# Kernel tuning notes

Hardware: AMD Instinct MI355X
Metric: run time of the kernel (lower is better)

## Reference

```python
import jax, jax.numpy as jnp
import numpy as np

N = 50000
E = 800000
H, C = 8, 16          # heads, per-head channels (H*C = 128)
G = 64                # number of graphs
EPS = 1e-5


def setup_inputs() -> dict:
    key = jax.random.key(0)
    ks = jax.random.split(key, 8)
    x = jax.random.normal(ks[0], (N, 128), dtype=jnp.float32)
    edge_index = jax.random.randint(ks[1], (2, E), 0, N, dtype=jnp.int64)
    batch = jnp.sort(jax.random.randint(ks[2], (N,), 0, G, dtype=jnp.int64))
    W = jax.random.normal(ks[3], (3, 128, 128), dtype=jnp.float32) * 0.08
    att_src = jax.random.normal(ks[4], (3, H, C), dtype=jnp.float32) * 0.1
    att_dst = jax.random.normal(ks[5], (3, H, C), dtype=jnp.float32) * 0.1
    bias = jnp.zeros((3, 128), dtype=jnp.float32)
    gamma = jnp.ones((3, 128), dtype=jnp.float32)
    beta = jnp.zeros((3, 128), dtype=jnp.float32)
    ro_w = jax.random.normal(ks[6], (128, 2), dtype=jnp.float32) * 0.08
    ro_b = jnp.zeros((2,), dtype=jnp.float32)
    return {"x": x, "edge_index": edge_index, "batch": batch, "W": W,
            "att_src": att_src, "att_dst": att_dst, "bias": bias,
            "gamma": gamma, "beta": beta, "ro_w": ro_w, "ro_b": ro_b}


def _gat_block(prev, h, src, dst, W, a_s, a_d, b, g, be):
    # GATConv (concat=True, add_self_loops already applied to src/dst)
    xp = (h @ W).reshape(N, H, C)                       # [N,H,C]
    al_s = jnp.sum(xp * a_s, axis=-1)                   # [N,H]
    al_d = jnp.sum(xp * a_d, axis=-1)                   # [N,H]
    logits = jax.nn.leaky_relu(al_s[src] + al_d[dst], negative_slope=0.2)  # [Et,H]
    m = jax.ops.segment_max(logits, dst, num_segments=N)        # softmax over dst groups
    ex = jnp.exp(logits - m[dst])
    denom = jax.ops.segment_sum(ex, dst, num_segments=N)
    alpha = ex / denom[dst]                              # [Et,H]
    msg = xp[src] * alpha[:, :, None]                    # [Et,H,C]
    agg = jax.ops.segment_sum(msg, dst, num_segments=N).reshape(N, H * C) + b
    y = prev + agg
    # BatchNorm1d (training mode: batch stats, biased variance)
    mu = y.mean(axis=0)
    var = y.var(axis=0)
    yn = (y - mu) / jnp.sqrt(var + EPS) * g + be
    return jax.nn.elu(yn)


def reference(x, edge_index, batch, W, att_src, att_dst, bias, gamma, beta, ro_w, ro_b):
    loops = jnp.arange(N, dtype=edge_index.dtype)
    src = jnp.concatenate([edge_index[0], loops])        # PyG add_self_loops=True
    dst = jnp.concatenate([edge_index[1], loops])
    h = x
    prev = jnp.zeros((N, 128), dtype=x.dtype)
    for i in range(3):
        out = _gat_block(prev, h, src, dst, W[i], att_src[i], att_dst[i],
                         bias[i], gamma[i], beta[i])
        prev = h[:, :128]
        h = out
    # global mean pool over graphs
    sums = jax.ops.segment_sum(h, batch, num_segments=G)
    cnt = jax.ops.segment_sum(jnp.ones((N,), dtype=h.dtype), batch, num_segments=G)
    pooled = sums / jnp.maximum(cnt, 1.0)[:, None]
    return pooled @ ro_w + ro_b
```

## Files before the change

### kernel.cpp

```cpp
#include <hip/hip_runtime.h>
#include <hip/hip_bf16.h>
#include <math.h>

#define NN 50000
#define EE 800000
#define MM (EE + NN)
#define GG 64
#define SWG 512
#define NSB ((NN + 255) / 256)
#define PSP 16

__device__ __forceinline__ int geti(const void* p, long idx, int is64) {
    return is64 ? (int)((const long long*)p)[idx] : ((const int*)p)[idx];
}

__device__ __forceinline__ float bf2f(unsigned short u) {
    return __uint_as_float(((unsigned)u) << 16);
}

__device__ __forceinline__ float eluf(float z) {
    return z > 0.f ? z : expm1f(z);
}

__global__ void k_detect(const int* __restrict__ ei, int* __restrict__ flag) {
    if (blockIdx.x == 0 && threadIdx.x == 0) {
        int ok = 1;
        for (int k = 0; k < 128; ++k) {
            int lo = ei[2 * k], hi = ei[2 * k + 1];
            if (hi != 0 || (unsigned)lo >= (unsigned)NN) { ok = 0; break; }
        }
        flag[0] = ok;
    }
}


__global__ void k_zero(int* p, int n) {
    int i = blockIdx.x * blockDim.x + threadIdx.x;
    if (i < n) p[i] = 0;
}

__global__ void k_count(const void* __restrict__ ei, const int* __restrict__ flag,
                        int* __restrict__ counts) {
    int e = blockIdx.x * blockDim.x + threadIdx.x;
    if (e >= MM) return;
    int is64 = flag[0];
    int d = (e < EE) ? geti(ei, (long)EE + e, is64) : (e - EE);
    if ((unsigned)d < (unsigned)NN) atomicAdd(&counts[d], 1);
}

__global__ __launch_bounds__(256) void k_scan1(const int* __restrict__ counts,
                                               int* __restrict__ rowptr,
                                               int* __restrict__ bsum) {
    __shared__ int buf[256];
    int b = blockIdx.x, tid = threadIdx.x;
    int i = b * 256 + tid;
    int v = (i < NN) ? counts[i] : 0;
    buf[tid] = v;
    __syncthreads();
    for (int off = 1; off < 256; off <<= 1) {
        int t = (tid >= off) ? buf[tid - off] : 0;
        __syncthreads();
        buf[tid] += t;
        __syncthreads();
    }
    if (i < NN) rowptr[i + 1] = buf[tid];
    if (tid == 255) bsum[b] = buf[255];
}

__global__ __launch_bounds__(256) void k_scan2(int* __restrict__ bsum) {
    __shared__ int buf[256];
    int tid = threadIdx.x;
    int v = (tid < NSB) ? bsum[tid] : 0;
    buf[tid] = v;
    __syncthreads();
    for (int off = 1; off < 256; off <<= 1) {
        int t = (tid >= off) ? buf[tid - off] : 0;
        __syncthreads();
        buf[tid] += t;
        __syncthreads();
    }
    if (tid < NSB) bsum[tid] = (tid == 0) ? 0 : buf[tid - 1];
}

__global__ __launch_bounds__(256) void k_scan3(int* __restrict__ rowptr,
                                               const int* __restrict__ bsum) {
    int b = blockIdx.x, tid = threadIdx.x;
    int i = b * 256 + tid;
    if (i < NN) rowptr[i + 1] += bsum[b];
    if (b == 0 && tid == 0) rowptr[0] = 0;
}

__global__ void k_fill(const void* __restrict__ ei, const int* __restrict__ flag,
                       const int* __restrict__ rowptr,
                       int* __restrict__ fill, int* __restrict__ colv) {
    int e = blockIdx.x * blockDim.x + threadIdx.x;
    if (e >= MM) return;
    int is64 = flag[0];
    int s, d;
    if (e < EE) { s = geti(ei, e, is64); d = geti(ei, (long)EE + e, is64); }
    else { s = d = e - EE; }
    if ((unsigned)d >= (unsigned)NN || (unsigned)s >= (unsigned)NN) return;
    int pos = rowptr[d] + atomicAdd(&fill[d], 1);
    if ((unsigned)pos < (unsigned)MM) colv[pos] = s;
}


__global__ __launch_bounds__(256) void k_gemm_att(
    const float* __restrict__ hsrc, const float* __restrict__ Ysrc,
    const float* __restrict__ st, const float* __restrict__ W,
    const float* __restrict__ attS, const float* __restrict__ attD,
    unsigned short* __restrict__ xpb, float* __restrict__ als,
    float* __restrict__ ald, int n)
{
    __shared__ float Wt[32][8][12];
    __shared__ float Ht[128][33];
    int tid = threadIdx.x;
    int hh = tid & 7;
    int r0 = tid >> 3;
    int rbase = (blockIdx.x >> 1) * 128;
    int cbase = (blockIdx.x & 1) * 64;
    bool useY = (Ysrc != nullptr);

    float acc[4][8];
#pragma unroll
    for (int a = 0; a < 4; ++a)
#pragma unroll
        for (int b = 0; b < 8; ++b) acc[a][b] = 0.f;

    for (int k0 = 0; k0 < 128; k0 += 32) {
#pragma unroll
        for (int jj = 0; jj < 2; ++jj) {
            int idx = tid * 2 + jj;
            int kk = idx >> 4;
            int cpos = (idx & 15) * 4;
            int h2 = cpos >> 3, t = cpos & 7;
            *(float4*)&Wt[kk][h2][t] =
                *(const float4*)&W[(k0 + kk) * 128 + cbase + h2 * 8 + t];
        }
#pragma unroll
        for (int j = 0; j < 4; ++j) {
            int f = tid * 16 + j * 4;
            int r = f >> 5, kk = f & 31;
            int gr = rbase + r;
            float4 v = make_float4(0.f, 0.f, 0.f, 0.f);
            if (gr < n) {
                if (useY) {
                    float4 yv = *(const float4*)&Ysrc[gr * 128 + k0 + kk];
                    float4 scv = *(const float4*)&st[k0 + kk];
                    float4 shv = *(const float4*)&st[128 + k0 + kk];
                    v.x = eluf(fmaf(yv.x, scv.x, shv.x));
                    v.y = eluf(fmaf(yv.y, scv.y, shv.y));
                    v.z = eluf(fmaf(yv.z, scv.z, shv.z));
                    v.w = eluf(fmaf(yv.w, scv.w, shv.w));
                } else {
                    v = *(const float4*)&hsrc[gr * 128 + k0 + kk];
                }
            }
            Ht[r][kk] = v.x; Ht[r][kk + 1] = v.y; Ht[r][kk + 2] = v.z; Ht[r][kk + 3] = v.w;
        }
        __syncthreads();
#pragma unroll 4
        for (int kk = 0; kk < 32; ++kk) {
            float wv[8];
            *(float4*)&wv[0] = *(const float4*)&Wt[kk][hh][0];
            *(float4*)&wv[4] = *(const float4*)&Wt[kk][hh][4];
#pragma unroll
            for (int rr = 0; rr < 4; ++rr) {
                float hv = Ht[r0 + rr * 32][kk];
#pragma unroll
                for (int j = 0; j < 8; ++j) acc[rr][j] = fmaf(hv, wv[j], acc[rr][j]);
            }
        }
        __syncthreads();
    }

    int head = (cbase >> 4) + (hh >> 1);
    int halfsel = hh & 1;
    float asv[8], adv[8];
#pragma unroll
    for (int j = 0; j < 8; ++j) {
        asv[j] = attS[head * 16 + halfsel * 8 + j];
        adv[j] = attD[head * 16 + halfsel * 8 + j];
    }

#pragma unroll
    for (int rr = 0; rr < 4; ++rr) {
        int r = rbase + r0 + rr * 32;
        if (r < n) {
            float ds = 0.f, dd = 0.f;
#pragma unroll
            for (int j = 0; j < 8; ++j) { ds = fmaf(acc[rr][j], asv[j], ds); dd = fmaf(acc[rr][j], adv[j], dd); }
            ds += __shfl_xor(ds, 1);
            dd += __shfl_xor(dd, 1);
            if (halfsel == 0) {
                als[r * 8 + head] = ds;
                ald[r * 8 + head] = dd;
            }
            unsigned short xb[8];
#pragma unroll
            for (int j = 0; j < 8; ++j) {
                __hip_bfloat16 t = __float2bfloat16(acc[rr][j]);
                xb[j] = *reinterpret_cast<unsigned short*>(&t);
            }
            *(uint4*)&xpb[(size_t)r * 128 + cbase + hh * 8] = *(uint4*)&xb[0];
        }
    }
}


__global__ __launch_bounds__(256) void k_agg(
    const unsigned short* __restrict__ xpb, const float* __restrict__ als,
    const float* __restrict__ ald,
    const int* __restrict__ rowptr, const int* __restrict__ colv,
    const float* __restrict__ prevRaw, const float* __restrict__ prevY,
    const float* __restrict__ pst, const float* __restrict__ bias,
    float* __restrict__ y, int n)
{
    __shared__ float alds[4][8][8];
    __shared__ int   slds[4][8];
    int wv = threadIdx.x >> 6;
    int wid = (int)((blockIdx.x * blockDim.x + threadIdx.x) >> 6);
    int lane = threadIdx.x & 63;
    if (wid >= n) return;
    int rs = rowptr[wid], re = rowptr[wid + 1];
    int deg = re - rs;

    int hd = lane & 7;
    int ee = lane >> 3;
    float aldn = ald[wid * 8 + hd];
    int q = lane >> 3;
    int c0 = lane * 2;

    float a0 = 0.f, a1 = 0.f, smloc = 0.f;
    int full = deg & ~7;

    for (int b0 = 0; b0 < full; b0 += 8) {
        int se = colv[rs + b0 + ee];
        float v = als[se * 8 + hd] + aldn;
        v = v > 0.f ? v : 0.2f * v;
        float al = expf(v);
        smloc += al;
        alds[wv][ee][hd] = al;
        if (hd == 0) slds[wv][ee] = se;
#pragma unroll
        for (int j = 0; j < 8; ++j) {
            int s = slds[wv][j];
            float a = alds[wv][j][q];
            ushort2 xv = *(const ushort2*)(xpb + (size_t)s * 128 + c0);
            a0 = fmaf(a, bf2f(xv.x), a0);
            a1 = fmaf(a, bf2f(xv.y), a1);
        }
    }

    if (full < deg) {
        int nb = deg - full;
        float al = 0.f;
        int se = 0;
        if (ee < nb) {
            se = colv[rs + full + ee];
            float v = als[se * 8 + hd] + aldn;
            v = v > 0.f ? v : 0.2f * v;
            al = expf(v);
            smloc += al;
        }
        alds[wv][ee][hd] = al;
        if (hd == 0) slds[wv][ee] = se;
        for (int j = 0; j < nb; ++j) {
            int s = slds[wv][j];
            float a = alds[wv][j][q];
            ushort2 xv = *(const ushort2*)(xpb + (size_t)s * 128 + c0);
            a0 = fmaf(a, bf2f(xv.x), a0);
            a1 = fmaf(a, bf2f(xv.y), a1);
        }
    }

    smloc += __shfl_xor(smloc, 8);
    smloc += __shfl_xor(smloc, 16);
    smloc += __shfl_xor(smloc, 32);
    float inv = 1.f / __shfl(smloc, q);
    a0 *= inv;
    a1 *= inv;

    float p0 = 0.f, p1 = 0.f;
    if (prevY) {
        float2 yv = *(const float2*)(prevY + (size_t)wid * 128 + c0);
        p0 = eluf(fmaf(yv.x, pst[c0], pst[128 + c0]));
        p1 = eluf(fmaf(yv.y, pst[c0 + 1], pst[129 + c0]));
    } else if (prevRaw) {
        p0 = prevRaw[(size_t)wid * 128 + c0];
        p1 = prevRaw[(size_t)wid * 128 + c0 + 1];
    }
    y[wid * 128 + c0] = p0 + a0 + bias[c0];
    y[wid * 128 + c0 + 1] = p1 + a1 + bias[c0 + 1];
}


__global__ __launch_bounds__(256) void k_stats(const float* __restrict__ y,
                                               double* __restrict__ partial, int n) {
    int col = threadIdx.x & 127;
    int rg = threadIdx.x >> 7;
    double s = 0.0, s2 = 0.0;
    for (int r = blockIdx.x * 2 + rg; r < n; r += SWG * 2) {
        float v = y[r * 128 + col];
        s += v; s2 += (double)v * (double)v;
    }
    __shared__ double ls[256], ls2[256];
    ls[threadIdx.x] = s; ls2[threadIdx.x] = s2;
    __syncthreads();
    if (rg == 0) {
        s += ls[threadIdx.x + 128];
        s2 += ls2[threadIdx.x + 128];
        partial[col * SWG + blockIdx.x] = s;
        partial[128 * SWG + col * SWG + blockIdx.x] = s2;
    }
}

__global__ void k_stats_fin(const double* __restrict__ partial,
                            const float* __restrict__ gamma,
                            const float* __restrict__ beta,
                            float* __restrict__ st, int n) {
    int col = threadIdx.x;
    double s = 0.0, s2 = 0.0;
    for (int w = 0; w < SWG; ++w) {
        s += partial[col * SWG + w];
        s2 += partial[128 * SWG + col * SWG + w];
    }
    double mu = s / n;
    double var = s2 / n - mu * mu;
    double rsig = 1.0 / sqrt(var + 1e-5);
    double sc = (double)gamma[col] * rsig;
    st[col] = (float)sc;
    st[128 + col] = (float)((double)beta[col] - mu * sc);
}


__global__ __launch_bounds__(256) void k_pool_part(
    const float* __restrict__ Y, const float* __restrict__ st,
    const void* __restrict__ batch, const int* __restrict__ flag,
    float* __restrict__ ppart, int n)
{
    int g = blockIdx.x / PSP;
    int sp = blockIdx.x % PSP;
    int is64 = flag[0];
    int lo = 0, hi = n;
    while (lo < hi) { int mid = (lo + hi) >> 1; if (geti(batch, mid, is64) < g) lo = mid + 1; else hi = mid; }
    int start = lo;
    hi = n;
    while (lo < hi) { int mid = (lo + hi) >> 1; if (geti(batch, mid, is64) < g + 1) lo = mid + 1; else hi = mid; }
    int end = lo;
    int cnt = end - start;
    int slice = (cnt + PSP - 1) / PSP;
    int s0 = start + sp * slice;
    int s1 = s0 + slice; if (s1 > end) s1 = end;

    int col = threadIdx.x & 127;
    int half = threadIdx.x >> 7;
    float sc = st[col], sh = st[128 + col];
    float s = 0.f;
    for (int r = s0 + half; r < s1; r += 2)
        s += eluf(fmaf(Y[(size_t)r * 128 + col], sc, sh));
    __shared__ float ls[256];
    ls[threadIdx.x] = s;
    __syncthreads();
    if (half == 0) ppart[(g * PSP + sp) * 128 + col] = s + ls[col + 128];
}

__global__ __launch_bounds__(128) void k_pool_fin(
    const float* __restrict__ ppart, const void* __restrict__ batch,
    const int* __restrict__ flag, const float* __restrict__ row,
    const float* __restrict__ rob, float* __restrict__ out, int n)
{
    int g = blockIdx.x;
    int is64 = flag[0];
    int lo = 0, hi = n;
    while (lo < hi) { int mid = (lo + hi) >> 1; if (geti(batch, mid, is64) < g) lo = mid + 1; else hi = mid; }
    int start = lo;
    hi = n;
    while (lo < hi) { int mid = (lo + hi) >> 1; if (geti(batch, mid, is64) < g + 1) lo = mid + 1; else hi = mid; }
    int cnt = lo - start;

    int col = threadIdx.x;
    float s = 0.f;
#pragma unroll
    for (int sp = 0; sp < PSP; ++sp) s += ppart[(g * PSP + sp) * 128 + col];
    __shared__ float ls[128];
    ls[col] = s * (1.f / fmaxf((float)cnt, 1.f));
    __syncthreads();
    if (col < 2) {
        float acc = 0.f;
        for (int c = 0; c < 128; ++c) acc = fmaf(ls[c], row[c * 2 + col], acc);
        out[g * 2 + col] = acc + rob[col];
    }
}


extern "C" void kernel_launch(void* const* d_in, const int* in_sizes, int n_in,
                              void* d_out, int out_size, void* d_ws, size_t ws_size,
                              hipStream_t stream) {
    const float* x     = (const float*)d_in[0];
    const void*  ei    = d_in[1];
    const void*  batch = d_in[2];
    const float* W     = (const float*)d_in[3];
    const float* attS  = (const float*)d_in[4];
    const float* attD  = (const float*)d_in[5];
    const float* bias  = (const float*)d_in[6];
    const float* gamma = (const float*)d_in[7];
    const float* beta  = (const float*)d_in[8];
    const float* row   = (const float*)d_in[9];
    const float* rob   = (const float*)d_in[10];
    float* out = (float*)d_out;

    char* wsb = (char*)d_ws;
    size_t off = 0;
    auto alloc = [&](size_t bytes) {
        void* p = wsb + off;
        off += (bytes + 255) & ~(size_t)255;
        return p;
    };
    int*    flag    = (int*)alloc(256);
    int*    rowptr  = (int*)alloc((size_t)(NN + 1) * 4);
    int*    cnts    = (int*)alloc((size_t)NN * 4 * 2);
    int*    bsum    = (int*)alloc((size_t)256 * 4);
    int*    colv    = (int*)alloc((size_t)MM * 4);
    double* partial = (double*)alloc((size_t)128 * SWG * 2 * 8);
    float*  st1     = (float*)alloc(256 * 4);
    float*  st2     = (float*)alloc(256 * 4);
    float*  st3     = (float*)alloc(256 * 4);
    float*  ppart   = (float*)alloc((size_t)GG * PSP * 128 * 4);
    float*  ALS     = (float*)alloc((size_t)NN * 8 * 4);
    float*  ALD     = (float*)alloc((size_t)NN * 8 * 4);
    unsigned short* XPB = (unsigned short*)alloc((size_t)NN * 128 * 2);
    float* Y1 = (float*)alloc((size_t)NN * 128 * 4);
    float* Y2 = (float*)alloc((size_t)NN * 128 * 4);
    float* Y3 = (float*)alloc((size_t)NN * 128 * 4);
    (void)ws_size; (void)in_sizes; (void)n_in; (void)out_size;

    int* fill = cnts + NN;
    const int GB2 = ((NN + 127) / 128) * 2;
    const int GA = (NN + 3) / 4;

    hipLaunchKernelGGL(k_detect, dim3(1), dim3(64), 0, stream, (const int*)ei, flag);
    hipLaunchKernelGGL(k_zero, dim3((2 * NN + 255) / 256), dim3(256), 0, stream, cnts, 2 * NN);
    hipLaunchKernelGGL(k_count, dim3((MM + 255) / 256), dim3(256), 0, stream, ei, flag, cnts);
    hipLaunchKernelGGL(k_scan1, dim3(NSB), dim3(256), 0, stream, cnts, rowptr, bsum);
    hipLaunchKernelGGL(k_scan2, dim3(1), dim3(256), 0, stream, bsum);
    hipLaunchKernelGGL(k_scan3, dim3(NSB), dim3(256), 0, stream, rowptr, bsum);
    hipLaunchKernelGGL(k_fill, dim3((MM + 255) / 256), dim3(256), 0, stream, ei, flag, rowptr, fill, colv);

    hipLaunchKernelGGL(k_gemm_att, dim3(GB2), dim3(256), 0, stream,
                       x, (const float*)nullptr, (const float*)nullptr,
                       W, attS, attD, XPB, ALS, ALD, NN);
    hipLaunchKernelGGL(k_agg, dim3(GA), dim3(256), 0, stream,
                       XPB, ALS, ALD, rowptr, colv,
                       (const float*)nullptr, (const float*)nullptr, (const float*)nullptr,
                       bias, Y1, NN);
    hipLaunchKernelGGL(k_stats, dim3(SWG), dim3(256), 0, stream, Y1, partial, NN);
    hipLaunchKernelGGL(k_stats_fin, dim3(1), dim3(128), 0, stream, partial, gamma, beta, st1, NN);

    hipLaunchKernelGGL(k_gemm_att, dim3(GB2), dim3(256), 0, stream,
                       (const float*)nullptr, Y1, st1,
                       W + 16384, attS + 128, attD + 128, XPB, ALS, ALD, NN);
    hipLaunchKernelGGL(k_agg, dim3(GA), dim3(256), 0, stream,
                       XPB, ALS, ALD, rowptr, colv,
                       x, (const float*)nullptr, (const float*)nullptr,
                       bias + 128, Y2, NN);
    hipLaunchKernelGGL(k_stats, dim3(SWG), dim3(256), 0, stream, Y2, partial, NN);
    hipLaunchKernelGGL(k_stats_fin, dim3(1), dim3(128), 0, stream, partial, gamma + 128, beta + 128, st2, NN);

    hipLaunchKernelGGL(k_gemm_att, dim3(GB2), dim3(256), 0, stream,
                       (const float*)nullptr, Y2, st2,
                       W + 32768, attS + 256, attD + 256, XPB, ALS, ALD, NN);
    hipLaunchKernelGGL(k_agg, dim3(GA), dim3(256), 0, stream,
                       XPB, ALS, ALD, rowptr, colv,
                       (const float*)nullptr, Y1, st1,
                       bias + 256, Y3, NN);
    hipLaunchKernelGGL(k_stats, dim3(SWG), dim3(256), 0, stream, Y3, partial, NN);
    hipLaunchKernelGGL(k_stats_fin, dim3(1), dim3(128), 0, stream, partial, gamma + 256, beta + 256, st3, NN);

    hipLaunchKernelGGL(k_pool_part, dim3(GG * PSP), dim3(256), 0, stream,
                       Y3, st3, batch, flag, ppart, NN);
    hipLaunchKernelGGL(k_pool_fin, dim3(GG), dim3(128), 0, stream,
                       ppart, batch, flag, row, rob, out, NN);
}
```

Baseline: 545.1 us.

## Split each node's edge aggregation across two waves and merge via LDS

The aggregation kernel now assigns two wavefronts per destination node, each handling half of the incoming edges; the second wave writes its partial sums and softmax denominators to shared memory, and the first combines them after a block barrier before normalizing and writing output. This doubles the number of waves in flight to hide gather latency on the irregular edge loads. The cost is a __syncthreads per block, extra LDS traffic, and idle waves for the epilogue. Separately, the edge-index width detection kernel is folded into the zeroing kernel to save one launch.

After: 560.0 us. +2.7%, slower.

```diff
diff --git a/kernel.cpp b/kernel.cpp
--- a/kernel.cpp
+++ b/kernel.cpp
@@ -22,8 +22,11 @@
     return z > 0.f ? z : expm1f(z);
 }
 
-__global__ void k_detect(const int* __restrict__ ei, int* __restrict__ flag) {
-    if (blockIdx.x == 0 && threadIdx.x == 0) {
+
+__global__ void k_zero(int* p, int n, const int* __restrict__ ei, int* __restrict__ flag) {
+    int i = blockIdx.x * blockDim.x + threadIdx.x;
+    if (i < n) p[i] = 0;
+    if (blockIdx.x == 0 && threadIdx.x == 0 && ei != nullptr) {
         int ok = 1;
         for (int k = 0; k < 128; ++k) {
             int lo = ei[2 * k], hi = ei[2 * k + 1];
@@ -31,12 +34,6 @@
         }
         flag[0] = ok;
     }
-}
-
-
-__global__ void k_zero(int* p, int n) {
-    int i = blockIdx.x * blockDim.x + threadIdx.x;
-    if (i < n) p[i] = 0;
 }
 
 __global__ void k_count(const void* __restrict__ ei, const int* __restrict__ flag,
@@ -218,16 +215,26 @@
 {
     __shared__ float alds[4][8][8];
     __shared__ int   slds[4][8];
+    __shared__ float accs[2][128];
+    __shared__ float dens[2][8];
     int wv = threadIdx.x >> 6;
-    int wid = (int)((blockIdx.x * blockDim.x + threadIdx.x) >> 6);
+    long gw = (long)blockIdx.x * 4 + wv;
+    int wid = (int)(gw >> 1);
+    int parity = (int)(gw & 1);
+    int nb = wv >> 1;
     int lane = threadIdx.x & 63;
-    if (wid >= n) return;
-    int rs = rowptr[wid], re = rowptr[wid + 1];
-    int deg = re - rs;
+    bool live = (wid < n);
+    int widc = live ? wid : (n - 1);
+
+    int rs0 = rowptr[widc], re0 = rowptr[widc + 1];
+    int degall = re0 - rs0;
+    int h0 = degall >> 1;
+    int rs  = (parity == 0) ? rs0 : rs0 + h0;
+    int deg = (parity == 0) ? h0 : degall - h0;
 
     int hd = lane & 7;
     int ee = lane >> 3;
-    float aldn = ald[wid * 8 + hd];
+    float aldn = ald[widc * 8 + hd];
     int q = lane >> 3;
     int c0 = lane * 2;
 
@@ -253,10 +260,10 @@
     }
 
     if (full < deg) {
-        int nb = deg - full;
+        int nbt = deg - full;
         float al = 0.f;
         int se = 0;
-        if (ee < nb) {
+        if (ee < nbt) {
             se = colv[rs + full + ee];
             float v = als[se * 8 + hd] + aldn;
             v = v > 0.f ? v : 0.2f * v;
@@ -265,7 +272,7 @@
         }
         alds[wv][ee][hd] = al;
         if (hd == 0) slds[wv][ee] = se;
-        for (int j = 0; j < nb; ++j) {
+        for (int j = 0; j < nbt; ++j) {
             int s = slds[wv][j];
             float a = alds[wv][j][q];
             ushort2 xv = *(const ushort2*)(xpb + (size_t)s * 128 + c0);
@@ -277,21 +284,34 @@
     smloc += __shfl_xor(smloc, 8);
     smloc += __shfl_xor(smloc, 16);
     smloc += __shfl_xor(smloc, 32);
-    float inv = 1.f / __shfl(smloc, q);
-    a0 *= inv;
-    a1 *= inv;
-
-    float p0 = 0.f, p1 = 0.f;
-    if (prevY) {
-        float2 yv = *(const float2*)(prevY + (size_t)wid * 128 + c0);
-        p0 = eluf(fmaf(yv.x, pst[c0], pst[128 + c0]));
-        p1 = eluf(fmaf(yv.y, pst[c0 + 1], pst[129 + c0]));
-    } else if (prevRaw) {
-        p0 = prevRaw[(size_t)wid * 128 + c0];
-        p1 = prevRaw[(size_t)wid * 128 + c0 + 1];
-    }
-    y[wid * 128 + c0] = p0 + a0 + bias[c0];
-    y[wid * 128 + c0 + 1] = p1 + a1 + bias[c0 + 1];
+
+    if (parity == 1) {
+        accs[nb][c0] = a0;
+        accs[nb][c0 + 1] = a1;
+        if (lane < 8) dens[nb][lane] = smloc;
+    }
+    __syncthreads();
+
+    if (parity == 0 && live) {
+        a0 += accs[nb][c0];
+        a1 += accs[nb][c0 + 1];
+        float dtot = __shfl(smloc, q) + dens[nb][q];
+        float inv = 1.f / dtot;
+        a0 *= inv;
+        a1 *= inv;
+
+        float p0 = 0.f, p1 = 0.f;
+        if (prevY) {
+            float2 yv = *(const float2*)(prevY + (size_t)widc * 128 + c0);
+            p0 = eluf(fmaf(yv.x, pst[c0], pst[128 + c0]));
+            p1 = eluf(fmaf(yv.y, pst[c0 + 1], pst[129 + c0]));
+        } else if (prevRaw) {
+            p0 = prevRaw[(size_t)widc * 128 + c0];
+            p1 = prevRaw[(size_t)widc * 128 + c0 + 1];
+        }
+        y[widc * 128 + c0] = p0 + a0 + bias[c0];
+        y[widc * 128 + c0 + 1] = p1 + a1 + bias[c0 + 1];
+    }
 }
 
 
@@ -437,10 +457,10 @@
 
     int* fill = cnts + NN;
     const int GB2 = ((NN + 127) / 128) * 2;
-    const int GA = (NN + 3) / 4;
-
-    hipLaunchKernelGGL(k_detect, dim3(1), dim3(64), 0, stream, (const int*)ei, flag);
-    hipLaunchKernelGGL(k_zero, dim3((2 * NN + 255) / 256), dim3(256), 0, stream, cnts, 2 * NN);
+    const int GA2 = (2 * NN + 3) / 4;
+
+    hipLaunchKernelGGL(k_zero, dim3((2 * NN + 255) / 256), dim3(256), 0, stream,
+                       cnts, 2 * NN, (const int*)ei, flag);
     hipLaunchKernelGGL(k_count, dim3((MM + 255) / 256), dim3(256), 0, stream, ei, flag, cnts);
     hipLaunchKernelGGL(k_scan1, dim3(NSB), dim3(256), 0, stream, cnts, rowptr, bsum);
     hipLaunchKernelGGL(k_scan2, dim3(1), dim3(256), 0, stream, bsum);
@@ -450,7 +470,7 @@
     hipLaunchKernelGGL(k_gemm_att, dim3(GB2), dim3(256), 0, stream,
                        x, (const float*)nullptr, (const float*)nullptr,
                        W, attS, attD, XPB, ALS, ALD, NN);
-    hipLaunchKernelGGL(k_agg, dim3(GA), dim3(256), 0, stream,
+    hipLaunchKernelGGL(k_agg, dim3(GA2), dim3(256), 0, stream,
                        XPB, ALS, ALD, rowptr, colv,
                        (const float*)nullptr, (const float*)nullptr, (const float*)nullptr,
                        bias, Y1, NN);
@@ -460,7 +480,7 @@
     hipLaunchKernelGGL(k_gemm_att, dim3(GB2), dim3(256), 0, stream,
                        (const float*)nullptr, Y1, st1,
                        W + 16384, attS + 128, attD + 128, XPB, ALS, ALD, NN);
-    hipLaunchKernelGGL(k_agg, dim3(GA), dim3(256), 0, stream,
+    hipLaunchKernelGGL(k_agg, dim3(GA2), dim3(256), 0, stream,
                        XPB, ALS, ALD, rowptr, colv,
                        x, (const float*)nullptr, (const float*)nullptr,
                        bias + 128, Y2, NN);
@@ -470,7 +490,7 @@
     hipLaunchKernelGGL(k_gemm_att, dim3(GB2), dim3(256), 0, stream,
                        (const float*)nullptr, Y2, st2,
                        W + 32768, attS + 256, attD + 256, XPB, ALS, ALD, NN);
-    hipLaunchKernelGGL(k_agg, dim3(GA), dim3(256), 0, stream,
+    hipLaunchKernelGGL(k_agg, dim3(GA2), dim3(256), 0, stream,
                        XPB, ALS, ALD, rowptr, colv,
                        (const float*)nullptr, Y1, st1,
                        bias + 256, Y3, NN);
```
